# Kernel optimization log

Measured on AMD Instinct MI355X. Metric: run time of the kernel, lower is better.

## Reference

```python
import jax, jax.numpy as jnp
from jax import lax
import numpy as np

N_SPLITS = 2
N_LEVELS = 3
B, T, C = 32, 1024, 128
HID = 512          # int(input_dim * hidden_size) = 128 * 4
K1, K2 = 5, 3      # first conv kernel_size, second conv kernel=3
N_INTER = 7        # 1 + 2 + 4 interactors in the binary tree
LEAKY_SLOPE = 0.01


def setup_inputs() -> dict:
    key = jax.random.key(0)
    ks = jax.random.split(key, 9)
    w = 0.05  # small init so exp-gating stays well-conditioned
    return {
        "x": jax.random.normal(ks[0], (B, T, C), jnp.float32),
        "mul_w1": jax.random.normal(ks[1], (N_INTER, N_SPLITS, K1, C, HID), jnp.float32) * w,
        "mul_b1": jnp.zeros((N_INTER, N_SPLITS, HID), jnp.float32),
        "mul_w2": jax.random.normal(ks[2], (N_INTER, N_SPLITS, K2, HID, C), jnp.float32) * w,
        "mul_b2": jnp.zeros((N_INTER, N_SPLITS, C), jnp.float32),
        "add_w1": jax.random.normal(ks[3], (N_INTER, N_SPLITS, K1, C, HID), jnp.float32) * w,
        "add_b1": jnp.zeros((N_INTER, N_SPLITS, HID), jnp.float32),
        "add_w2": jax.random.normal(ks[4], (N_INTER, N_SPLITS, K2, HID, C), jnp.float32) * w,
        "add_b2": jnp.zeros((N_INTER, N_SPLITS, C), jnp.float32),
    }


def _leaky(x):
    return jnp.where(x > 0, x, LEAKY_SLOPE * x)


def _causal_conv(x, w, b):
    # x: [B, L, Cin], w: [K, Cin, Cout] (keras WIO layout); 'causal' = left-pad K-1
    k = w.shape[0]
    y = lax.conv_general_dilated(x, w, window_strides=(1,),
                                 padding=[(k - 1, 0)],
                                 dimension_numbers=("NWC", "WIO", "NWC"))
    return y + b


def _conv_seq(x, w1, b1, w2, b2):
    # Conv1D(causal, LeakyReLU 0.01) -> Dropout(identity at inference) -> Conv1D(k=3, causal, tanh)
    h = _leaky(_causal_conv(x, w1, b1))
    return jnp.tanh(_causal_conv(h, w2, b2))


def _interactor(x, idx, p):
    # x: [B, L, C]; strided temporal split into N_SPLITS pieces of length L//N_SPLITS
    splits = [x[:, i::N_SPLITS, :] for i in range(N_SPLITS)]
    scale = N_SPLITS - 1
    mul_list = []
    for i in range(N_SPLITS):
        s = 0.0
        for j in range(N_SPLITS):
            if j != i:
                s = s + _conv_seq(splits[j], p["mul_w1"][idx, i], p["mul_b1"][idx, i],
                                  p["mul_w2"][idx, i], p["mul_b2"][idx, i])
        # prod_j exp(f(x_j)) ** (1/scale) == exp(sum_j f(x_j) / scale)
        mul_list.append(splits[i] * jnp.exp(s / scale))
    out = []
    for i in range(N_SPLITS):
        a = 0.0
        for j in range(N_SPLITS):
            if j != i:
                a = a + _conv_seq(mul_list[j], p["add_w1"][idx, i], p["add_b1"][idx, i],
                                  p["add_w2"][idx, i], p["add_b2"][idx, i])
        a = a / scale
        out.append(mul_list[i] + a if i % 2 == 0 else mul_list[i] - a)
    return out


def reference(x, mul_w1, mul_b1, mul_w2, mul_b2, add_w1, add_b1, add_w2, add_b2):
    p = {"mul_w1": mul_w1, "mul_b1": mul_b1, "mul_w2": mul_w2, "mul_b2": mul_b2,
         "add_w1": add_w1, "add_b1": add_b1, "add_w2": add_w2, "add_b2": add_b2}
    t_in = x.shape[1]
    min_unit = N_SPLITS ** N_LEVELS
    pad = (-t_in) % min_unit  # left zero-pad to a multiple of n_splits**n_levels
    xp = jnp.pad(x, ((0, 0), (pad, 0), (0, 0)))
    seq = [xp]
    idx = 0
    for lvl in range(N_LEVELS):
        nxt = []
        for j in range(N_SPLITS ** lvl):
            nxt += _interactor(seq[j], idx, p)
            idx += 1
        seq = nxt
    # rev_split: recursively concatenate along time with stride `steps`
    while len(seq) > 1:
        steps = len(seq) // N_SPLITS
        seq = [jnp.concatenate([seq[i + s * steps] for s in range(N_SPLITS)], axis=1)
               for i in range(steps)]
    return seq[0][:, -t_in:, :]
```

## Files before the change

### kernel.cpp

```cpp
#include <hip/hip_runtime.h>
#include <hip/hip_bf16.h>
#include <stdint.h>


static constexpr int B_ = 32, T_ = 1024, C_ = 128, HID_ = 512;
static constexpr int K1_ = 5, K2_ = 3;

typedef __attribute__((ext_vector_type(8))) _Float16 half8;
typedef __attribute__((ext_vector_type(4))) float f32x4;

__device__ __forceinline__ unsigned short f2h(float f) {
    _Float16 h = (_Float16)f;
    return __builtin_bit_cast(unsigned short, h);
}

__device__ __forceinline__ float h2f(unsigned short u) {
    return (float)__builtin_bit_cast(_Float16, u);
}

__device__ __forceinline__ void gload16(const void* g, void* l) {
    __builtin_amdgcn_global_load_lds(
        (const __attribute__((address_space(1))) unsigned int*)g,
        (__attribute__((address_space(3))) unsigned int*)l, 16, 0, 0);
}

template<int CIN, int COUT, bool SWZ>
__global__ __launch_bounds__(256)
void wprep_k(const float* __restrict__ win1, unsigned short* __restrict__ wout1,
             const float* __restrict__ win2, unsigned short* __restrict__ wout2,
             int nhalf) {
    constexpr int TA = CIN / 64, TB = COUT / 64;
    int blk = blockIdx.x;
    int tb = blk % TB;
    int ta = (blk / TB) % TA;
    int s  = blk / (TA * TB);
    const float* win;
    unsigned short* wout;
    if (s < nhalf) { win = win1; wout = wout1; }
    else           { win = win2; wout = wout2; s -= nhalf; }
    __shared__ float tile[64][65];
    const float* src = win + (size_t)s * CIN * COUT;
    unsigned short* dst = wout + (size_t)s * CIN * COUT;
    int cl = threadIdx.x & 63;
    int rw = threadIdx.x >> 6;
    for (int r = rw; r < 64; r += 4)
        tile[r][cl] = src[(size_t)(ta * 64 + r) * COUT + tb * 64 + cl];
    __syncthreads();
    for (int r = rw; r < 64; r += 4) {
        int co = tb * 64 + r;
        int ci = ta * 64 + cl;
        int ciw = SWZ ? ((ci & ~127) | ((ci & 127) ^ ((co & 7) << 3))) : ci;
        dst[(size_t)co * CIN + ciw] = f2h(tile[cl][r]);
    }
}

__global__ __launch_bounds__(256)
void split_k(const float* __restrict__ cur, unsigned short* __restrict__ outb,
             int Ls) {
    int idx = blockIdx.x * 256 + threadIdx.x;
    int row = idx >> 5;
    int cq  = (idx & 31) << 2;
    int BLs = B_ * Ls;
    int g  = row / BLs;
    int r2 = row - g * BLs;
    int b  = r2 / Ls;
    int u  = r2 - b * Ls;
    int p = g >> 1, i = g & 1;
    const float4 v = *(const float4*)(cur +
        ((size_t)(p * B_ + b) * (2 * Ls) + 2 * u + i) * C_ + cq);
    ushort4 o;
    o.x = f2h(v.x); o.y = f2h(v.y); o.z = f2h(v.z); o.w = f2h(v.w);
    int cqw = cq ^ (((u + 4) & 7) << 3);
    *(ushort4*)(outb + (size_t)row * C_ + cqw) = o;
}

__global__ __launch_bounds__(256, 2)
void conv1_k(const unsigned short* __restrict__ actb,
             const unsigned short* __restrict__ wL,
             const float* __restrict__ bias,
             unsigned short* __restrict__ hid,
             const unsigned short* __restrict__ zp,
             int Ls, int rsplit, int idxbase) {
    __shared__ unsigned short smemA[2][80 * 128];

    const int tid = threadIdx.x;
    const int lane = tid & 63;
    const int w = tid >> 6;
    const int wr = w >> 1, wc = w & 1;

    const int blk = blockIdx.x;
    const int ct = blk & 7;
    const int rs = (blk >> 3) % rsplit;
    const int g  = (blk >> 3) / rsplit;
    const int n0 = ct * 64;
    const int gin  = g ^ 1;
    const int widx = (idxbase + (g >> 1)) * 2 + (g & 1);

    const char* gbase = (const char*)(actb + (size_t)gin * B_ * Ls * C_);
    const float* bptr = bias + (size_t)widx * HID_;

    const unsigned short* wlane = wL + (size_t)widx * (K1_ * HID_ * C_)
        + (size_t)(n0 + wc * 32 + (lane & 15)) * C_ + ((lane >> 4) << 3);
    half8 breg[K1_][2][4];
#pragma unroll
    for (int t = 0; t < K1_; ++t)
#pragma unroll
        for (int n = 0; n < 2; ++n)
#pragma unroll
            for (int ks = 0; ks < 4; ++ks)
                breg[t][n][ks] = *(const half8*)(wlane
                    + ((size_t)t * HID_ + n * 16) * C_ + ks * 32);

    const float bv0 = bptr[n0 + wc * 32 + (lane & 15)];
    const float bv1 = bptr[n0 + wc * 32 + 16 + (lane & 15)];

    const int rtbase = rs * 8;
    const int i0 = ct & 7;

    auto stage = [&](int rt, int p) {
        const int b  = (rt * 64) / Ls;
        const int t0 = (rt * 64) % Ls;
        const char* inb = gbase + (size_t)b * Ls * 256;
#pragma unroll
        for (int j = 0; j < 5; ++j) {
            int ch = w * 5 + j;
            int q = ch * 1024 + lane * 16;
            int r = q >> 8;
            int cb = q & 255;
            int t = t0 - 4 + r;
            const char* src = (t >= 0) ? inb + (size_t)t * 256 + cb
                                       : (const char*)zp + cb;
            gload16(src, (char*)smemA[p] + ch * 1024);
        }
    };

    stage(rtbase + i0, 0);
    asm volatile("s_waitcnt vmcnt(0)" ::: "memory");
    __syncthreads();

#pragma unroll
    for (int i = 0; i < 8; ++i) {
        const int rt = rtbase + ((i + i0) & 7);
        const int b  = (rt * 64) / Ls;
        const int t0 = (rt * 64) % Ls;
        const int p  = i & 1;

        __syncthreads();
        if (i < 7) stage(rtbase + ((i + 1 + i0) & 7), p ^ 1);
        if (i > 0) {
            if (i < 7) {
                asm volatile("s_waitcnt vmcnt(21)" ::: "memory");
            } else {
                asm volatile("s_waitcnt vmcnt(16)" ::: "memory");
            }
            __syncthreads();
        }

        f32x4 acc[2][2];
#pragma unroll
        for (int m = 0; m < 2; ++m)
#pragma unroll
            for (int n = 0; n < 2; ++n) acc[m][n] = (f32x4){0.f, 0.f, 0.f, 0.f};

        const unsigned short* sA = smemA[p];
#pragma unroll
        for (int kk = 0; kk < K1_; ++kk) {
#pragma unroll
            for (int ks = 0; ks < 4; ++ks) {
                half8 aF[2];
                const int cole = ks * 32 + ((lane >> 4) << 3);
#pragma unroll
                for (int m = 0; m < 2; ++m) {
                    int ar = kk + wr * 32 + m * 16 + (lane & 15);
                    aF[m] = *(const half8*)(sA + ar * 128 + (cole ^ ((ar & 7) << 3)));
                }
#pragma unroll
                for (int m = 0; m < 2; ++m) {
                    acc[m][0] = __builtin_amdgcn_mfma_f32_16x16x32_f16(
                        aF[m], breg[kk][0][ks], acc[m][0], 0, 0, 0);
                    acc[m][1] = __builtin_amdgcn_mfma_f32_16x16x32_f16(
                        aF[m], breg[kk][1][ks], acc[m][1], 0, 0, 0);
                }
            }
        }

        unsigned short* outp = hid + ((size_t)(g * B_ + b) * Ls + t0) * HID_;
#pragma unroll
        for (int n = 0; n < 2; ++n) {
            const int co = n0 + wc * 32 + n * 16 + (lane & 15);
            const float bv = n ? bv1 : bv0;
#pragma unroll
            for (int m = 0; m < 2; ++m) {
                const int u0 = wr * 32 + m * 16 + ((lane >> 4) << 2);
#pragma unroll
                for (int q = 0; q < 4; ++q) {
                    float v = acc[m][n][q] + bv;
                    v = (v > 0.f) ? v : 0.01f * v;
                    int t = t0 + u0 + q;
                    int cow = (co & ~127) | ((co & 127) ^ (((t + 2) & 7) << 3));
                    outp[(size_t)(u0 + q) * HID_ + cow] = f2h(v);
                }
            }
        }
    }
}

template<int EPI>
__global__ __launch_bounds__(256, 3)
void conv2_k(const unsigned short* __restrict__ hid,
             const unsigned short* __restrict__ wT,
             const float* __restrict__ bias,
             const unsigned short* __restrict__ ain,
             const unsigned short* __restrict__ gate,
             unsigned short* __restrict__ gout,
             unsigned short* __restrict__ actn,
             float* __restrict__ dout,
             const unsigned short* __restrict__ zp,
             int Ls, int RT, int idxbase) {
    __shared__ unsigned short smemA[66 * 128];
    __shared__ unsigned short smemB[128 * 128];

    const int tid = threadIdx.x;
    const int lane = tid & 63;
    const int w = tid >> 6;
    const int wr = w >> 1, wc = w & 1;

    int blk = blockIdx.x;
    const int rt = blk % RT;
    const int g  = blk / RT;
    const int rowstart = rt * 64;
    const int b  = rowstart / Ls;
    const int t0 = rowstart - b * Ls;
    const int widx = (idxbase + (g >> 1)) * 2 + (g & 1);

    const char* inb = (const char*)(hid + (size_t)(g * B_ + b) * Ls * HID_);
    const char* wb  = (const char*)(wT + (size_t)widx * (K2_ * C_ * HID_));
    const float* bptr = bias + (size_t)widx * C_;

    const int c0 = blk & 3;
    const int k0 = blk % 3;

    f32x4 acc[2][4];
#pragma unroll
    for (int m = 0; m < 2; ++m)
#pragma unroll
        for (int n = 0; n < 4; ++n) acc[m][n] = (f32x4){0.f, 0.f, 0.f, 0.f};

    for (int ckp = 0; ckp < 4; ++ckp) {
        const int ck = (ckp + c0) & 3;
        if (ckp) __syncthreads();
        for (int ch = w; ch < 17; ch += 4) {
            int q = ch * 1024 + lane * 16;
            if (q < 16896) {
                int r = q >> 8;
                int cb = q & 255;
                int t = t0 - 2 + r;
                const char* src = (t >= 0)
                    ? inb + (size_t)t * 1024 + ck * 256 + cb
                    : (const char*)zp + cb;
                gload16(src, (char*)smemA + ch * 1024);
            }
        }
        for (int kkp = 0; kkp < K2_; ++kkp) {
            const int kk = (kkp + k0) % 3;
            if (kkp) __syncthreads();
            const char* wt = wb + (size_t)kk * C_ * HID_ * 2;
            for (int ch = w; ch < 32; ch += 4) {
                int q = ch * 1024 + lane * 16;
                int co = q >> 8;
                int cb = q & 255;
                gload16(wt + (size_t)co * 1024 + ck * 256 + cb,
                        (char*)smemB + ch * 1024);
            }
            asm volatile("s_waitcnt vmcnt(0)" ::: "memory");
            __syncthreads();

#pragma unroll
            for (int ks = 0; ks < 4; ++ks) {
                half8 aF[2], bF[4];
                const int cole = ks * 32 + ((lane >> 4) << 3);
#pragma unroll
                for (int m = 0; m < 2; ++m) {
                    int ar = kk + wr * 32 + m * 16 + (lane & 15);
                    aF[m] = *(const half8*)(smemA + ar * 128 + (cole ^ ((ar & 7) << 3)));
                }
#pragma unroll
                for (int n = 0; n < 4; ++n) {
                    int br = wc * 64 + n * 16 + (lane & 15);
                    bF[n] = *(const half8*)(smemB + br * 128 + (cole ^ ((br & 7) << 3)));
                }
#pragma unroll
                for (int m = 0; m < 2; ++m)
#pragma unroll
                    for (int n = 0; n < 4; ++n)
                        acc[m][n] = __builtin_amdgcn_mfma_f32_16x16x32_f16(
                            aF[m], bF[n], acc[m][n], 0, 0, 0);
            }
        }
    }

    const size_t rowb = (size_t)(g * B_ + b) * Ls + t0;
    const int Ls2 = Ls >> 1;
    const int i_ = g & 1;
#pragma unroll
    for (int n = 0; n < 4; ++n) {
        int c = wc * 64 + n * 16 + (lane & 15);
        float bv = bptr[c];
#pragma unroll
        for (int m = 0; m < 2; ++m) {
            int u0 = wr * 32 + m * 16 + ((lane >> 4) << 2);
#pragma unroll
            for (int q = 0; q < 4; ++q) {
                float v = acc[m][n][q] + bv;
                float xc = fminf(fmaxf(v, -15.f), 15.f);
                float e2 = __expf(2.f * xc);
                float th = (e2 - 1.f) / (e2 + 1.f);
                size_t ro = rowb + (size_t)(u0 + q);
                int u = t0 + u0 + q;
                int cw = c ^ (((u + 4) & 7) << 3);
                if (EPI == 0) {
                    float sv = h2f(ain[ro * C_ + cw]);
                    float mv = sv * __expf(th);
                    gout[ro * C_ + cw] = f2h(mv);
                } else {
                    float mv = h2f(gate[ro * C_ + cw]);
                    float val = (i_ == 0) ? (mv + th) : (mv - th);
                    if (EPI == 1) {
                        int gq = g * 2 + (u & 1);
                        int uq = u >> 1;
                        int cw2 = c ^ (((uq + 4) & 7) << 3);
                        actn[((size_t)(gq * B_ + b) * Ls2 + uq) * C_ + cw2] = f2h(val);
                    } else {
                        int tau = u | (((g >> 2) & 1) << 7) | (((g >> 1) & 1) << 8)
                                    | ((g & 1) << 9);
                        dout[((size_t)b * T_ + tau) * C_ + c] = val;
                    }
                }
            }
        }
    }
}

extern "C" void kernel_launch(void* const* d_in, const int* in_sizes, int n_in,
                              void* d_out, int out_size, void* d_ws, size_t ws_size,
                              hipStream_t stream) {
    const float* x   = (const float*)d_in[0];
    const float* mw1 = (const float*)d_in[1];
    const float* mb1 = (const float*)d_in[2];
    const float* mw2 = (const float*)d_in[3];
    const float* mb2 = (const float*)d_in[4];
    const float* aw1 = (const float*)d_in[5];
    const float* ab1 = (const float*)d_in[6];
    const float* aw2 = (const float*)d_in[7];
    const float* ab2 = (const float*)d_in[8];

    char* ws = (char*)d_ws;
    size_t off = 0;
    auto alloc = [&](size_t sz) {
        char* p = ws + off;
        off += (sz + 255) & ~(size_t)255;
        return p;
    };
    unsigned short* zp   = (unsigned short*)alloc(8192);
    unsigned short* w1m  = (unsigned short*)alloc((size_t)14 * 5 * 512 * 128 * 2);
    unsigned short* w1a  = (unsigned short*)alloc((size_t)14 * 5 * 512 * 128 * 2);
    unsigned short* w2m  = (unsigned short*)alloc((size_t)14 * 3 * 128 * 512 * 2);
    unsigned short* w2a  = (unsigned short*)alloc((size_t)14 * 3 * 128 * 512 * 2);
    unsigned short* actb = (unsigned short*)alloc((size_t)4194304 * 2);
    unsigned short* actg = (unsigned short*)alloc((size_t)4194304 * 2);
    unsigned short* hidb = (unsigned short*)alloc((size_t)16777216 * 2);
    (void)ws_size; (void)n_in; (void)in_sizes; (void)out_size;

    hipMemsetAsync(zp, 0, 8192, stream);

    wprep_k<128, 512, false><<<2240, 256, 0, stream>>>(mw1, w1m, aw1, w1a, 70);
    wprep_k<512, 128, true ><<<1344, 256, 0, stream>>>(mw2, w2m, aw2, w2a, 42);

    split_k<<<4096, 256, 0, stream>>>(x, actb, 512);

    for (int lvl = 0; lvl < 3; ++lvl) {
        const int G = 2 << lvl;
        const int Ls = (1024 >> lvl) >> 1;
        const int idxbase = (1 << lvl) - 1;
        const int rsplit = (B_ * Ls / 64) / 8;
        const int RT2 = Ls / 2;

        conv1_k<<<512, 256, 0, stream>>>(actb, w1m, mb1, hidb, zp,
                                         Ls, rsplit, idxbase);
        conv2_k<0><<<G * RT2, 256, 0, stream>>>(hidb, w2m, mb2, actb, nullptr,
                                                actg, nullptr, nullptr,
                                                zp, Ls, RT2, idxbase);
        conv1_k<<<512, 256, 0, stream>>>(actg, w1a, ab1, hidb, zp,
                                         Ls, rsplit, idxbase);
        if (lvl < 2) {
            conv2_k<1><<<G * RT2, 256, 0, stream>>>(hidb, w2a, ab2, nullptr, actg,
                                                    nullptr, actb, nullptr,
                                                    zp, Ls, RT2, idxbase);
        } else {
            conv2_k<2><<<G * RT2, 256, 0, stream>>>(hidb, w2a, ab2, nullptr, actg,
                                                    nullptr, nullptr, (float*)d_out,
                                                    zp, Ls, RT2, idxbase);
        }
    }
}
```

Measured before the change: 359.8 us.

## Double conv2 row tile to 128 with 512-thread blocks sharing weight tiles

The second-conv kernel now processes 128 time rows per block with 8 waves instead of 64 rows with 4 waves, so each staged weight tile in LDS is reused across twice as many rows and grid size halves. The activation tile is loaded once per channel chunk, and B/A staging are merged into one barrier phase per kernel tap. This cuts global weight traffic and barrier count, but raises LDS use per block and lowers the occupancy bound to 2 blocks of 512 threads. A t<Ls guard is added for the halo rows.

```diff
diff --git a/kernel.cpp b/kernel.cpp
--- a/kernel.cpp
+++ b/kernel.cpp
@@ -206,7 +206,7 @@
 }
 
 template<int EPI>
-__global__ __launch_bounds__(256, 3)
+__global__ __launch_bounds__(512, 2)
 void conv2_k(const unsigned short* __restrict__ hid,
              const unsigned short* __restrict__ wT,
              const float* __restrict__ bias,
@@ -217,18 +217,20 @@
              float* __restrict__ dout,
              const unsigned short* __restrict__ zp,
              int Ls, int RT, int idxbase) {
-    __shared__ unsigned short smemA[66 * 128];
+    __shared__ unsigned short smemA[132 * 128];
     __shared__ unsigned short smemB[128 * 128];
 
     const int tid = threadIdx.x;
     const int lane = tid & 63;
     const int w = tid >> 6;
-    const int wr = w >> 1, wc = w & 1;
+    const int wr = w & 3, wc = w >> 2;
+    const int hi8 = (lane >> 4) << 3;
+    const int l15 = lane & 15;
 
     int blk = blockIdx.x;
     const int rt = blk % RT;
     const int g  = blk / RT;
-    const int rowstart = rt * 64;
+    const int rowstart = rt * 128;
     const int b  = rowstart / Ls;
     const int t0 = rowstart - b * Ls;
     const int widx = (idxbase + (g >> 1)) * 2 + (g & 1);
@@ -240,53 +242,63 @@
     const int c0 = blk & 3;
     const int k0 = blk % 3;
 
-    f32x4 acc[2][4];
-#pragma unroll
-    for (int m = 0; m < 2; ++m)
-#pragma unroll
-        for (int n = 0; n < 4; ++n) acc[m][n] = (f32x4){0.f, 0.f, 0.f, 0.f};
-
-    for (int ckp = 0; ckp < 4; ++ckp) {
-        const int ck = (ckp + c0) & 3;
-        if (ckp) __syncthreads();
-        for (int ch = w; ch < 17; ch += 4) {
-            int q = ch * 1024 + lane * 16;
-            if (q < 16896) {
+    auto stageA = [&](int ck) {
+#pragma unroll
+        for (int j = 0; j < 5; ++j) {
+            int ch = w + j * 8;
+            if (ch < 33) {
+                int q = ch * 1024 + lane * 16;
                 int r = q >> 8;
                 int cb = q & 255;
                 int t = t0 - 2 + r;
-                const char* src = (t >= 0)
+                const char* src = (t >= 0 && t < Ls)
                     ? inb + (size_t)t * 1024 + ck * 256 + cb
                     : (const char*)zp + cb;
                 gload16(src, (char*)smemA + ch * 1024);
             }
         }
+    };
+    auto stageB = [&](int ck, int kk) {
+        const char* wt = wb + (size_t)kk * C_ * HID_ * 2;
+#pragma unroll
+        for (int j = 0; j < 4; ++j) {
+            int ch = w * 4 + j;
+            int q = ch * 1024 + lane * 16;
+            int co = q >> 8;
+            int cb = q & 255;
+            gload16(wt + (size_t)co * 1024 + ck * 256 + cb,
+                    (char*)smemB + ch * 1024);
+        }
+    };
+
+    f32x4 acc[2][4];
+#pragma unroll
+    for (int m = 0; m < 2; ++m)
+#pragma unroll
+        for (int n = 0; n < 4; ++n) acc[m][n] = (f32x4){0.f, 0.f, 0.f, 0.f};
+
+    for (int ckp = 0; ckp < 4; ++ckp) {
+        const int ck = (ckp + c0) & 3;
         for (int kkp = 0; kkp < K2_; ++kkp) {
             const int kk = (kkp + k0) % 3;
-            if (kkp) __syncthreads();
-            const char* wt = wb + (size_t)kk * C_ * HID_ * 2;
-            for (int ch = w; ch < 32; ch += 4) {
-                int q = ch * 1024 + lane * 16;
-                int co = q >> 8;
-                int cb = q & 255;
-                gload16(wt + (size_t)co * 1024 + ck * 256 + cb,
-                        (char*)smemB + ch * 1024);
-            }
+            if (ckp | kkp) __syncthreads();
+            stageB(ck, kk);
+            if (kkp == 0) stageA(ck);
             asm volatile("s_waitcnt vmcnt(0)" ::: "memory");
             __syncthreads();
 
 #pragma unroll
             for (int ks = 0; ks < 4; ++ks) {
                 half8 aF[2], bF[4];
-                const int cole = ks * 32 + ((lane >> 4) << 3);
+                const int cole = ks * 32 + hi8;
 #pragma unroll
                 for (int m = 0; m < 2; ++m) {
-                    int ar = kk + wr * 32 + m * 16 + (lane & 15);
+                    int ar = kk + wr * 32 + m * 16 + l15;
                     aF[m] = *(const half8*)(smemA + ar * 128 + (cole ^ ((ar & 7) << 3)));
                 }
 #pragma unroll
                 for (int n = 0; n < 4; ++n) {
-                    int br = wc * 64 + n * 16 + (lane & 15);
+                    int br = wc * 64 + n * 16 + l15;
                     bF[n] = *(const half8*)(smemB + br * 128 + (cole ^ ((br & 7) << 3)));
                 }
 #pragma unroll
@@ -304,7 +316,7 @@
     const int i_ = g & 1;
 #pragma unroll
     for (int n = 0; n < 4; ++n) {
-        int c = wc * 64 + n * 16 + (lane & 15);
+        int c = wc * 64 + n * 16 + l15;
         float bv = bptr[c];
 #pragma unroll
         for (int m = 0; m < 2; ++m) {
@@ -383,21 +395,21 @@
         const int Ls = (1024 >> lvl) >> 1;
         const int idxbase = (1 << lvl) - 1;
         const int rsplit = (B_ * Ls / 64) / 8;
-        const int RT2 = Ls / 2;
+        const int RT2 = B_ * Ls / 128;
 
         conv1_k<<<512, 256, 0, stream>>>(actb, w1m, mb1, hidb, zp,
                                          Ls, rsplit, idxbase);
-        conv2_k<0><<<G * RT2, 256, 0, stream>>>(hidb, w2m, mb2, actb, nullptr,
+        conv2_k<0><<<G * RT2, 512, 0, stream>>>(hidb, w2m, mb2, actb, nullptr,
                                                 actg, nullptr, nullptr,
                                                 zp, Ls, RT2, idxbase);
         conv1_k<<<512, 256, 0, stream>>>(actg, w1a, ab1, hidb, zp,
                                          Ls, rsplit, idxbase);
         if (lvl < 2) {
-            conv2_k<1><<<G * RT2, 256, 0, stream>>>(hidb, w2a, ab2, nullptr, actg,
+            conv2_k<1><<<G * RT2, 512, 0, stream>>>(hidb, w2a, ab2, nullptr, actg,
                                                     nullptr, actb, nullptr,
                                                     zp, Ls, RT2, idxbase);
         } else {
-            conv2_k<2><<<G * RT2, 256, 0, stream>>>(hidb, w2a, ab2, nullptr, actg,
+            conv2_k<2><<<G * RT2, 512, 0, stream>>>(hidb, w2a, ab2, nullptr, actg,
                                                     nullptr, nullptr, (float*)d_out,
                                                     zp, Ls, RT2, idxbase);
         }
```

New measurement: 366.5 us. No clear change (+1.9%).
